# Optimization experiments

Measured on AMD Instinct MI355X. Metric: run time of the kernel, lower is better.

The kernel has to match this reference:

```python
import jax, jax.numpy as jnp
import numpy as np

B, M, N = 8, 8192, 8192  # batch, input neurons, output neurons
SPIKE_CAP = 0.9          # VPRTempo caps spike amplitude at 0.9


def setup_inputs() -> dict:
    key = jax.random.key(0)
    k0, k1, k2, k3 = jax.random.split(key, 4)
    # pre-synaptic spike amplitudes in [0, 1)
    pre_spikes = jax.random.uniform(k0, (B, 1, M), dtype=jnp.float32)
    # combined excitatory+inhibitory weights
    W = jax.random.normal(k1, (M, N), dtype=jnp.float32) * 0.01
    # per-neuron thresholds, uniform in thr_range = [0, 0.5]
    thr = jax.random.uniform(k2, (B, 1, N), dtype=jnp.float32) * 0.5
    # per-neuron constant input, uniform in const_inp = [0, 0.1]
    const_inp = jax.random.uniform(k3, (B, 1, N), dtype=jnp.float32) * 0.1
    return {"pre_spikes": pre_spikes, "W": W, "thr": thr, "const_inp": const_inp}


def reference(pre_spikes, W, thr, const_inp):
    # membrane potential: weighted pre-synaptic spikes + constant input
    x = jnp.einsum('bom,mn->bon', pre_spikes, W) + const_inp  # [B,1,N]
    # spike generation: amplitude above threshold, clamped to [0, 0.9]
    spikes = jnp.clip(x - thr, 0.0, SPIKE_CAP)
    return spikes
```

## Files before the change

### kernel.cpp

```cpp
#include <hip/hip_runtime.h>


constexpr int Mdim = 8192;
constexpr int Ndim = 8192;
constexpr int Bdim = 8;
constexpr int KCH  = 64;
constexpr int ROWS = Mdim / KCH;
constexpr int TILE_N = 1024;
constexpr float CAP = 0.9f;

__global__ __launch_bounds__(256, 2) void snn_stage1(
    const float* __restrict__ pre,
    const float* __restrict__ W,
    float* __restrict__ part)
{
    const int t   = threadIdx.x;
    const int col = blockIdx.x * TILE_N + t * 4;
    const int r0  = blockIdx.y * ROWS;

    float4 acc[Bdim];
#pragma unroll
    for (int b = 0; b < Bdim; ++b) acc[b] = make_float4(0.f, 0.f, 0.f, 0.f);

    for (int r = r0; r < r0 + ROWS; r += 8) {
        float4 w[8];
#pragma unroll
        for (int j = 0; j < 8; ++j)
            w[j] = *reinterpret_cast<const float4*>(W + (size_t)(r + j) * Ndim + col);

        float4 pA[Bdim], pB[Bdim];
#pragma unroll
        for (int b = 0; b < Bdim; ++b) {
            pA[b] = *reinterpret_cast<const float4*>(pre + b * Mdim + r);
            pB[b] = *reinterpret_cast<const float4*>(pre + b * Mdim + r + 4);
        }

#pragma unroll
        for (int b = 0; b < Bdim; ++b) {
            float4 a = acc[b];
            a.x = fmaf(pA[b].x, w[0].x, a.x); a.y = fmaf(pA[b].x, w[0].y, a.y);
            a.z = fmaf(pA[b].x, w[0].z, a.z); a.w = fmaf(pA[b].x, w[0].w, a.w);
            a.x = fmaf(pA[b].y, w[1].x, a.x); a.y = fmaf(pA[b].y, w[1].y, a.y);
            a.z = fmaf(pA[b].y, w[1].z, a.z); a.w = fmaf(pA[b].y, w[1].w, a.w);
            a.x = fmaf(pA[b].z, w[2].x, a.x); a.y = fmaf(pA[b].z, w[2].y, a.y);
            a.z = fmaf(pA[b].z, w[2].z, a.z); a.w = fmaf(pA[b].z, w[2].w, a.w);
            a.x = fmaf(pA[b].w, w[3].x, a.x); a.y = fmaf(pA[b].w, w[3].y, a.y);
            a.z = fmaf(pA[b].w, w[3].z, a.z); a.w = fmaf(pA[b].w, w[3].w, a.w);
            a.x = fmaf(pB[b].x, w[4].x, a.x); a.y = fmaf(pB[b].x, w[4].y, a.y);
            a.z = fmaf(pB[b].x, w[4].z, a.z); a.w = fmaf(pB[b].x, w[4].w, a.w);
            a.x = fmaf(pB[b].y, w[5].x, a.x); a.y = fmaf(pB[b].y, w[5].y, a.y);
            a.z = fmaf(pB[b].y, w[5].z, a.z); a.w = fmaf(pB[b].y, w[5].w, a.w);
            a.x = fmaf(pB[b].z, w[6].x, a.x); a.y = fmaf(pB[b].z, w[6].y, a.y);
            a.z = fmaf(pB[b].z, w[6].z, a.z); a.w = fmaf(pB[b].z, w[6].w, a.w);
            a.x = fmaf(pB[b].w, w[7].x, a.x); a.y = fmaf(pB[b].w, w[7].y, a.y);
            a.z = fmaf(pB[b].w, w[7].z, a.z); a.w = fmaf(pB[b].w, w[7].w, a.w);
            acc[b] = a;
        }
    }

    float* pslice = part + (size_t)blockIdx.y * (Bdim * Ndim);
#pragma unroll
    for (int b = 0; b < Bdim; ++b)
        *reinterpret_cast<float4*>(pslice + (size_t)b * Ndim + col) = acc[b];
}

__global__ __launch_bounds__(256, 4) void snn_stage2(
    const float* __restrict__ part,
    const float* __restrict__ thr,
    const float* __restrict__ cst,
    float* __restrict__ out)
{
    const int i = blockIdx.x * 256 + threadIdx.x;
    float s = 0.f;
#pragma unroll
    for (int k = 0; k < KCH; ++k)
        s += part[(size_t)k * (Bdim * Ndim) + i];
    float x = s + cst[i] - thr[i];
    x = fminf(fmaxf(x, 0.f), CAP);
    out[i] = x;
}

extern "C" void kernel_launch(void* const* d_in, const int* in_sizes, int n_in,
                              void* d_out, int out_size, void* d_ws, size_t ws_size,
                              hipStream_t stream) {
    const float* pre = (const float*)d_in[0];
    const float* W   = (const float*)d_in[1];
    const float* thr = (const float*)d_in[2];
    const float* cst = (const float*)d_in[3];
    float* out  = (float*)d_out;
    float* part = (float*)d_ws;

    dim3 g1(Ndim / TILE_N, KCH);
    hipLaunchKernelGGL(snn_stage1, g1, dim3(256), 0, stream, pre, W, part);

    dim3 g2((Bdim * Ndim) / 256);
    hipLaunchKernelGGL(snn_stage2, g2, dim3(256), 0, stream, part, thr, cst, out);
}
```

Measured before the change: 379.0 us.

## Stage pre-spikes in LDS, widen column tiles, stagger row order across blocks

Stage 1 now gives each block two 1024-column halves of a 2048-column panel over a 64-row chunk, with 128 K-chunks instead of 64. The pre-spike values for the chunk are staged once in shared memory rather than reloaded from global per row group. Row iteration is phase-rotated per block, and stage 2 rotates its chunk order, to spread accesses across memory channels. The cost is twice the partial-sum workspace traffic and more accumulator registers per thread, which may hurt occupancy.

```diff
diff --git a/kernel.cpp b/kernel.cpp
--- a/kernel.cpp
+++ b/kernel.cpp
@@ -4,9 +4,10 @@
 constexpr int Mdim = 8192;
 constexpr int Ndim = 8192;
 constexpr int Bdim = 8;
-constexpr int KCH  = 64;
-constexpr int ROWS = Mdim / KCH;
-constexpr int TILE_N = 1024;
+constexpr int PANELS  = 4;
+constexpr int PANEL_N = Ndim / PANELS;
+constexpr int CHUNKS  = 128;
+constexpr int CROWS   = Mdim / CHUNKS;
 constexpr float CAP = 0.9f;
 
 __global__ __launch_bounds__(256, 2) void snn_stage1(
@@ -14,54 +15,78 @@
     const float* __restrict__ W,
     float* __restrict__ part)
 {
-    const int t   = threadIdx.x;
-    const int col = blockIdx.x * TILE_N + t * 4;
-    const int r0  = blockIdx.y * ROWS;
+    __shared__ float lds_pre[Bdim * CROWS];
 
-    float4 acc[Bdim];
+    const int t     = threadIdx.x;
+    const int panel = blockIdx.x;
+    const int chunk = blockIdx.y;
+    const int r0    = chunk * CROWS;
+    const int colA  = panel * PANEL_N + t * 4;
+    const int colB  = colA + 1024;
+
+    for (int q = t; q < Bdim * CROWS; q += 256) {
+        int b = q >> 6, j = q & 63;
+        lds_pre[q] = pre[b * Mdim + r0 + j];
+    }
+    __syncthreads();
+
+    float4 accA[Bdim], accB[Bdim];
 #pragma unroll
-    for (int b = 0; b < Bdim; ++b) acc[b] = make_float4(0.f, 0.f, 0.f, 0.f);
+    for (int b = 0; b < Bdim; ++b) {
+        accA[b] = make_float4(0.f, 0.f, 0.f, 0.f);
+        accB[b] = make_float4(0.f, 0.f, 0.f, 0.f);
+    }
 
-    for (int r = r0; r < r0 + ROWS; r += 8) {
-        float4 w[8];
+    const int phase = (blockIdx.y * 5 + blockIdx.x) & 15;
+    for (int i = 0; i < 16; ++i) {
+        const int rr = ((i + phase) & 15) * 4;
+        const int r  = r0 + rr;
+
+        float4 wA[4], wB[4];
 #pragma unroll
-        for (int j = 0; j < 8; ++j)
-            w[j] = *reinterpret_cast<const float4*>(W + (size_t)(r + j) * Ndim + col);
+        for (int j = 0; j < 4; ++j) {
+            const float* row = W + (size_t)(r + j) * Ndim;
+            wA[j] = *reinterpret_cast<const float4*>(row + colA);
+            wB[j] = *reinterpret_cast<const float4*>(row + colB);
+        }
 
-        float4 pA[Bdim], pB[Bdim];
+        float4 pf[Bdim];
 #pragma unroll
-        for (int b = 0; b < Bdim; ++b) {
-            pA[b] = *reinterpret_cast<const float4*>(pre + b * Mdim + r);
-            pB[b] = *reinterpret_cast<const float4*>(pre + b * Mdim + r + 4);
-        }
+        for (int b = 0; b < Bdim; ++b)
+            pf[b] = *reinterpret_cast<const float4*>(lds_pre + b * CROWS + rr);
 
 #pragma unroll
         for (int b = 0; b < Bdim; ++b) {
-            float4 a = acc[b];
-            a.x = fmaf(pA[b].x, w[0].x, a.x); a.y = fmaf(pA[b].x, w[0].y, a.y);
-            a.z = fmaf(pA[b].x, w[0].z, a.z); a.w = fmaf(pA[b].x, w[0].w, a.w);
-            a.x = fmaf(pA[b].y, w[1].x, a.x); a.y = fmaf(pA[b].y, w[1].y, a.y);
-            a.z = fmaf(pA[b].y, w[1].z, a.z); a.w = fmaf(pA[b].y, w[1].w, a.w);
-            a.x = fmaf(pA[b].z, w[2].x, a.x); a.y = fmaf(pA[b].z, w[2].y, a.y);
-            a.z = fmaf(pA[b].z, w[2].z, a.z); a.w = fmaf(pA[b].z, w[2].w, a.w);
-            a.x = fmaf(pA[b].w, w[3].x, a.x); a.y = fmaf(pA[b].w, w[3].y, a.y);
-            a.z = fmaf(pA[b].w, w[3].z, a.z); a.w = fmaf(pA[b].w, w[3].w, a.w);
-            a.x = fmaf(pB[b].x, w[4].x, a.x); a.y = fmaf(pB[b].x, w[4].y, a.y);
-            a.z = fmaf(pB[b].x, w[4].z, a.z); a.w = fmaf(pB[b].x, w[4].w, a.w);
-            a.x = fmaf(pB[b].y, w[5].x, a.x); a.y = fmaf(pB[b].y, w[5].y, a.y);
-            a.z = fmaf(pB[b].y, w[5].z, a.z); a.w = fmaf(pB[b].y, w[5].w, a.w);
-            a.x = fmaf(pB[b].z, w[6].x, a.x); a.y = fmaf(pB[b].z, w[6].y, a.y);
-            a.z = fmaf(pB[b].z, w[6].z, a.z); a.w = fmaf(pB[b].z, w[6].w, a.w);
-            a.x = fmaf(pB[b].w, w[7].x, a.x); a.y = fmaf(pB[b].w, w[7].y, a.y);
-            a.z = fmaf(pB[b].w, w[7].z, a.z); a.w = fmaf(pB[b].w, w[7].w, a.w);
-            acc[b] = a;
+            float4 a = accA[b], c = accB[b];
+            a.x = fmaf(pf[b].x, wA[0].x, a.x); a.y = fmaf(pf[b].x, wA[0].y, a.y);
+            a.z = fmaf(pf[b].x, wA[0].z, a.z); a.w = fmaf(pf[b].x, wA[0].w, a.w);
+            c.x = fmaf(pf[b].x, wB[0].x, c.x); c.y = fmaf(pf[b].x, wB[0].y, c.y);
+            c.z = fmaf(pf[b].x, wB[0].z, c.z); c.w = fmaf(pf[b].x, wB[0].w, c.w);
+
+            a.x = fmaf(pf[b].y, wA[1].x, a.x); a.y = fmaf(pf[b].y, wA[1].y, a.y);
+            a.z = fmaf(pf[b].y, wA[1].z, a.z); a.w = fmaf(pf[b].y, wA[1].w, a.w);
+            c.x = fmaf(pf[b].y, wB[1].x, c.x); c.y = fmaf(pf[b].y, wB[1].y, c.y);
+            c.z = fmaf(pf[b].y, wB[1].z, c.z); c.w = fmaf(pf[b].y, wB[1].w, c.w);
+
+            a.x = fmaf(pf[b].z, wA[2].x, a.x); a.y = fmaf(pf[b].z, wA[2].y, a.y);
+            a.z = fmaf(pf[b].z, wA[2].z, a.z); a.w = fmaf(pf[b].z, wA[2].w, a.w);
+            c.x = fmaf(pf[b].z, wB[2].x, c.x); c.y = fmaf(pf[b].z, wB[2].y, c.y);
+            c.z = fmaf(pf[b].z, wB[2].z, c.z); c.w = fmaf(pf[b].z, wB[2].w, c.w);
+
+            a.x = fmaf(pf[b].w, wA[3].x, a.x); a.y = fmaf(pf[b].w, wA[3].y, a.y);
+            a.z = fmaf(pf[b].w, wA[3].z, a.z); a.w = fmaf(pf[b].w, wA[3].w, a.w);
+            c.x = fmaf(pf[b].w, wB[3].x, c.x); c.y = fmaf(pf[b].w, wB[3].y, c.y);
+            c.z = fmaf(pf[b].w, wB[3].z, c.z); c.w = fmaf(pf[b].w, wB[3].w, c.w);
+            accA[b] = a; accB[b] = c;
         }
     }
 
-    float* pslice = part + (size_t)blockIdx.y * (Bdim * Ndim);
+    float* ps = part + (size_t)chunk * (Bdim * Ndim);
 #pragma unroll
-    for (int b = 0; b < Bdim; ++b)
-        *reinterpret_cast<float4*>(pslice + (size_t)b * Ndim + col) = acc[b];
+    for (int b = 0; b < Bdim; ++b) {
+        *reinterpret_cast<float4*>(ps + (size_t)b * Ndim + colA) = accA[b];
+        *reinterpret_cast<float4*>(ps + (size_t)b * Ndim + colB) = accB[b];
+    }
 }
 
 __global__ __launch_bounds__(256, 4) void snn_stage2(
@@ -70,11 +95,14 @@
     const float* __restrict__ cst,
     float* __restrict__ out)
 {
-    const int i = blockIdx.x * 256 + threadIdx.x;
+    const int bid = blockIdx.x;
+    const int i = bid * 256 + threadIdx.x;
     float s = 0.f;
-#pragma unroll
-    for (int k = 0; k < KCH; ++k)
-        s += part[(size_t)k * (Bdim * Ndim) + i];
+#pragma unroll 8
+    for (int k = 0; k < CHUNKS; ++k) {
+        int kk = (k + bid) & (CHUNKS - 1);
+        s += part[(size_t)kk * (Bdim * Ndim) + i];
+    }
     float x = s + cst[i] - thr[i];
     x = fminf(fmaxf(x, 0.f), CAP);
     out[i] = x;
@@ -90,7 +118,7 @@
     float* out  = (float*)d_out;
     float* part = (float*)d_ws;
 
-    dim3 g1(Ndim / TILE_N, KCH);
+    dim3 g1(PANELS, CHUNKS);
     hipLaunchKernelGGL(snn_stage1, g1, dim3(256), 0, stream, pre, W, part);
 
     dim3 g2((Bdim * Ndim) / 256);
```

After: 368.1 us. 2.9% less time.
